# Kernel optimization log

Measured on AMD Instinct MI355X. Metric: run time of the kernel, lower is better.

Reference implementation:

```python
import jax, jax.numpy as jnp
import numpy as np

B, S, D, H = 4, 1024, 1024, 16
DH = D // H
RD = float(np.sqrt(D))


def linear_vdp(mu_a, var_a, mu_b, var_b):
    # Product of two independent random matrices: E[AB], Var[AB] (elementwise)
    mean = mu_a @ mu_b
    var = var_a @ var_b + var_a @ (mu_b ** 2) + (mu_a ** 2) @ var_b
    return mean, var


def softmax_vdp(a, var_a):
    # p = softmax(a); variance via squared Jacobian J_ij = p_i(delta_ij - p_j):
    # var_out_i = p_i^2 * (sum_j p_j^2 var_j + var_i * (1 - 2 p_i))
    p = jax.nn.softmax(a, axis=-1)
    s = jnp.sum(p * p * var_a, axis=-1, keepdims=True)
    var_out = p * p * (s + var_a * (1.0 - 2.0 * p))
    return p, var_out


def setup_inputs() -> dict:
    key = jax.random.key(0)
    ks = jax.random.split(key, 8)
    x = jax.random.normal(ks[0], (B, S, D), dtype=jnp.float32)
    var_x = jax.random.uniform(ks[1], (B, S, D), dtype=jnp.float32) * 0.1
    k = jax.random.normal(ks[2], (B, H, S, DH), dtype=jnp.float32)
    var_k = jax.random.uniform(ks[3], (B, H, S, DH), dtype=jnp.float32) * 0.1
    v = jax.random.normal(ks[4], (B, H, S, DH), dtype=jnp.float32)
    var_v = jax.random.uniform(ks[5], (B, H, S, DH), dtype=jnp.float32) * 0.1
    # LinearVDP(d, d, bias=False): weight mean + (positive) weight variance
    Wq_mu = jax.random.normal(ks[6], (D, D), dtype=jnp.float32) / np.sqrt(D)
    Wq_var = jax.random.uniform(ks[7], (D, D), dtype=jnp.float32) * (0.1 / D)
    return {"x": x, "var_x": var_x, "k": k, "var_k": var_k, "v": v,
            "var_v": var_v, "Wq_mu": Wq_mu, "Wq_var": Wq_var}


def reference(x, var_x, k, var_k, v, var_v, Wq_mu, Wq_var):
    # LinearVDP projection (y = x W^T with random weight)
    q = x @ Wq_mu.T
    var_q = var_x @ Wq_var.T + var_x @ (Wq_mu ** 2).T + (x ** 2) @ Wq_var.T
    # split heads: [B,S,D] -> [B,H,S,DH]
    q = q.reshape(B, S, H, DH).transpose(0, 2, 1, 3)
    var_q = var_q.reshape(B, S, H, DH).transpose(0, 2, 1, 3)
    # scores with variance propagation
    a, var_a = linear_vdp(q, var_q, jnp.swapaxes(k, 2, 3), jnp.swapaxes(var_k, 2, 3))
    a = a / RD
    var_a = var_a / (RD ** 2)
    # causal mask (-inf above diagonal) on the mean path only
    causal = jnp.triu(jnp.ones((S, S), dtype=bool), k=1)
    a = jnp.where(causal, -jnp.inf, a)
    a, var_a = softmax_vdp(a, var_a)
    # attention * values with variance propagation
    a, var_a = linear_vdp(a, var_a, v, var_v)
    # merge heads: [B,H,S,DH] -> [B,S,D]
    a = a.transpose(0, 2, 1, 3).reshape(B, S, D)
    var_a = var_a.transpose(0, 2, 1, 3).reshape(B, S, D)
    return x + a, var_a
```

## Files before the change

kernel.cpp:

```cpp
#include <hip/hip_runtime.h>
#include <hip/hip_bf16.h>
#include <math.h>

#define NB 4
#define NS 1024
#define ND 1024
#define NH 16
#define NDH 64
#define M4 4194304
#define M1 1048576

typedef float f16v __attribute__((ext_vector_type(16)));
typedef short bf8 __attribute__((ext_vector_type(8)));
typedef unsigned short ushort_t;

union U8 { bf8 v; unsigned u[4]; unsigned short s[8]; };

__device__ __forceinline__ unsigned pk(float lo, float hi) {
    __hip_bfloat162 h2 = __float22bfloat162_rn(make_float2(lo, hi));
    return *reinterpret_cast<unsigned*>(&h2);
}
__device__ __forceinline__ unsigned short f2b(float f) {
    unsigned u = __float_as_uint(f);
    unsigned r = (u + 0x7fffu + ((u >> 16) & 1u)) >> 16;
    return (unsigned short)r;
}
__device__ __forceinline__ float b2f(unsigned short h) {
    return __uint_as_float(((unsigned)h) << 16);
}
__device__ __forceinline__ f16v zero16() {
    f16v z;
    #pragma unroll
    for (int i = 0; i < 16; ++i) z[i] = 0.f;
    return z;
}
__device__ __forceinline__ void vscale(f16v& v, float s) {
    #pragma unroll
    for (int i = 0; i < 16; ++i) v[i] *= s;
}

__device__ __forceinline__ void gl_lds16(const ushort_t* g, ushort_t* l) {
    __builtin_amdgcn_global_load_lds(
        (const __attribute__((address_space(1))) unsigned int*)g,
        (__attribute__((address_space(3))) unsigned int*)l,
        16, 0, 0);
}

__device__ __forceinline__ bf8 mkB(unsigned p0, unsigned p1, unsigned p2, unsigned p3, int h) {
    unsigned own0 = h ? p2 : p0;
    unsigned own1 = h ? p3 : p1;
    unsigned ct0  = h ? p0 : p2;
    unsigned ct1  = h ? p1 : p3;
    unsigned x0 = (unsigned)__shfl_xor((int)ct0, 32);
    unsigned x1 = (unsigned)__shfl_xor((int)ct1, 32);
    U8 B;
    B.u[0] = h ? x0 : own0;
    B.u[1] = h ? x1 : own1;
    B.u[2] = h ? own0 : x0;
    B.u[3] = h ? own1 : x1;
    return B.v;
}


__global__ __launch_bounds__(256)
void prep_all(const float* __restrict__ x, const float* __restrict__ vx,
              const float* __restrict__ K,  const float* __restrict__ VK,
              const float* __restrict__ Vv, const float* __restrict__ VV,
              const float* __restrict__ Wm, const float* __restrict__ Wv,
              ushort_t* __restrict__ kmF, ushort_t* __restrict__ k2F, ushort_t* __restrict__ kvF,
              ushort_t* __restrict__ vmF, ushort_t* __restrict__ wF,  ushort_t* __restrict__ vvF,
              ushort_t* __restrict__ fx, ushort_t* __restrict__ fvx, ushort_t* __restrict__ fx2,
              ushort_t* __restrict__ fm, ushort_t* __restrict__ fw2, ushort_t* __restrict__ fv)
{
    __shared__ ushort_t Lm[2048], Lw[2048], Lv[2048];
    const int tid = threadIdx.x;
    const int bid = blockIdx.x;

    if (bid < 2048) {
        const int bh = bid >> 5, s = bid & 31;
        const int jp  = tid >> 3;
        const int dh0 = (tid & 7) * 8;
        const size_t gin = ((size_t)bh * NS + s * 32 + jp) * NDH + dh0;
        const size_t sbase = ((size_t)bh * 32 + s) * 2048;

        float kk[8], uu[8], vm[8], vv[8];
        *(float4*)(kk)   = *(const float4*)(K  + gin); *(float4*)(kk+4) = *(const float4*)(K  + gin + 4);
        *(float4*)(uu)   = *(const float4*)(VK + gin); *(float4*)(uu+4) = *(const float4*)(VK + gin + 4);
        *(float4*)(vm)   = *(const float4*)(Vv + gin); *(float4*)(vm+4) = *(const float4*)(Vv + gin + 4);
        *(float4*)(vv)   = *(const float4*)(VV + gin); *(float4*)(vv+4) = *(const float4*)(VV + gin + 4);

        const size_t kout = sbase + (size_t)((tid & 7) >> 1) * 512
                          + (jp + 32 * ((tid & 7) & 1)) * 8;
        unsigned o0[4], o1[4], o2[4];
        #pragma unroll
        for (int t = 0; t < 4; ++t) {
            o0[t] = pk(kk[2*t], kk[2*t+1]);
            o1[t] = pk(fmaf(kk[2*t],kk[2*t],uu[2*t]), fmaf(kk[2*t+1],kk[2*t+1],uu[2*t+1]));
            o2[t] = pk(uu[2*t], uu[2*t+1]);
        }
        *(uint4*)(kmF + kout) = make_uint4(o0[0],o0[1],o0[2],o0[3]);
        *(uint4*)(k2F + kout) = make_uint4(o1[0],o1[1],o1[2],o1[3]);
        *(uint4*)(kvF + kout) = make_uint4(o2[0],o2[1],o2[2],o2[3]);

        #pragma unroll
        for (int e = 0; e < 8; ++e) {
            const int dh = dh0 + e;
            const int idx = ((dh >> 5) * 2 + (jp >> 4)) * 512
                          + ((dh & 31) + 32 * ((jp >> 3) & 1)) * 8 + (jp & 7);
            Lm[idx] = f2b(vm[e]);
            Lw[idx] = f2b(fmaf(vm[e], vm[e], vv[e]));
            Lv[idx] = f2b(vv[e]);
        }
        __syncthreads();
        const size_t vout = sbase + (size_t)tid * 8;
        *(uint4*)(vmF + vout) = *(const uint4*)(Lm + tid * 8);
        *(uint4*)(wF  + vout) = *(const uint4*)(Lw + tid * 8);
        *(uint4*)(vvF + vout) = *(const uint4*)(Lv + tid * 8);
    } else {
        const size_t g = (size_t)(bid - 2048) * 256 + tid;
        if (g < 524288) {
            const size_t g0 = g * 8;
            const int row = (int)(g0 >> 10), k0 = (int)(g0 & 1023);
            const size_t fo = ((size_t)(row >> 5) * 64 + (k0 >> 4)) * 512
                            + ((row & 31) + 32 * ((k0 >> 3) & 1)) * 8;
            float a[8], c[8];
            *(float4*)(a)   = *(const float4*)(x + g0);  *(float4*)(a+4) = *(const float4*)(x + g0 + 4);
            *(float4*)(c)   = *(const float4*)(vx + g0); *(float4*)(c+4) = *(const float4*)(vx + g0 + 4);
            *(uint4*)(fx  + fo) = make_uint4(pk(a[0],a[1]), pk(a[2],a[3]), pk(a[4],a[5]), pk(a[6],a[7]));
            *(uint4*)(fvx + fo) = make_uint4(pk(c[0],c[1]), pk(c[2],c[3]), pk(c[4],c[5]), pk(c[6],c[7]));
            *(uint4*)(fx2 + fo) = make_uint4(pk(a[0]*a[0],a[1]*a[1]), pk(a[2]*a[2],a[3]*a[3]),
                                             pk(a[4]*a[4],a[5]*a[5]), pk(a[6]*a[6],a[7]*a[7]));
        } else {
            const size_t g0 = (g - 524288) * 8;
            const int row = (int)(g0 >> 10), k0 = (int)(g0 & 1023);
            const size_t fo = ((size_t)(row >> 5) * 64 + (k0 >> 4)) * 512
                            + ((row & 31) + 32 * ((k0 >> 3) & 1)) * 8;
            float a[8], c[8];
            *(float4*)(a)   = *(const float4*)(Wm + g0); *(float4*)(a+4) = *(const float4*)(Wm + g0 + 4);
            *(float4*)(c)   = *(const float4*)(Wv + g0); *(float4*)(c+4) = *(const float4*)(Wv + g0 + 4);
            *(uint4*)(fm  + fo) = make_uint4(pk(a[0],a[1]), pk(a[2],a[3]), pk(a[4],a[5]), pk(a[6],a[7]));
            *(uint4*)(fv  + fo) = make_uint4(pk(c[0],c[1]), pk(c[2],c[3]), pk(c[4],c[5]), pk(c[6],c[7]));
            *(uint4*)(fw2 + fo) = make_uint4(pk(fmaf(a[0],a[0],c[0]), fmaf(a[1],a[1],c[1])),
                                             pk(fmaf(a[2],a[2],c[2]), fmaf(a[3],a[3],c[3])),
                                             pk(fmaf(a[4],a[4],c[4]), fmaf(a[5],a[5],c[5])),
                                             pk(fmaf(a[6],a[6],c[6]), fmaf(a[7],a[7],c[7])));
        }
    }
}

__global__ __launch_bounds__(256, 2)
void qproj_b(const ushort_t* __restrict__ xplanes,
             const ushort_t* __restrict__ wplanes,
             ushort_t* __restrict__ qmF, ushort_t* __restrict__ vqF)
{
    __shared__ ushort_t wstg[3][12 * 512];

    const int tid  = threadIdx.x;
    const int w    = tid >> 6;
    const int lane = tid & 63;
    const int lh   = lane & 31;
    const int h    = lane >> 5;
    const int head = blockIdx.x;
    const int mb   = blockIdx.y;
    const int mt   = mb * 4 + w;
    const int nt   = head * 2 + (w & 1);

    f16v aQ0 = zero16(), aQ1 = zero16(), aV0 = zero16(), aV1 = zero16();

    const ushort_t* xb = xplanes + (size_t)mt * 64 * 512 + lane * 8;
    const ushort_t* wsrc = wplanes + ((size_t)nt * 64 + (w >> 1)) * 512 + lane * 8;

    #pragma unroll
    for (int q = 0; q < 3; ++q)
        gl_lds16(wsrc + (size_t)q * M1, &wstg[0][(3 * w + q) * 512 + lane * 8]);
    #pragma unroll
    for (int q = 0; q < 3; ++q)
        gl_lds16(wsrc + (size_t)q * M1 + 2 * 512, &wstg[1][(3 * w + q) * 512 + lane * 8]);

    for (int t = 0; t < 32; ++t) {
        const int cur = t % 3;
        if (t + 2 < 32) {
            const int nxt = (t + 2) % 3;
            #pragma unroll
            for (int q = 0; q < 3; ++q)
                gl_lds16(wsrc + (size_t)q * M1 + (size_t)(2 * (t + 2)) * 512,
                         &wstg[nxt][(3 * w + q) * 512 + lane * 8]);
            asm volatile("s_waitcnt vmcnt(6)" ::: "memory");
        } else if (t + 1 < 32) {
            asm volatile("s_waitcnt vmcnt(3)" ::: "memory");
        } else {
            asm volatile("s_waitcnt vmcnt(0)" ::: "memory");
        }
        __builtin_amdgcn_s_barrier();
        __builtin_amdgcn_sched_barrier(0);

        const ushort_t* sc = wstg[cur];
        #pragma unroll
        for (int kcL = 0; kcL < 2; ++kcL) {
            const int off = (2 * t + kcL) * 512;
            bf8 bx  = *(const bf8*)(xb + 0 * (size_t)M4 + off);
            bf8 bvx = *(const bf8*)(xb + 1 * (size_t)M4 + off);
            bf8 bx2 = *(const bf8*)(xb + 2 * (size_t)M4 + off);
            bf8 A0m = *(const bf8*)(sc + (3 * (2 * kcL + 0) + 0) * 512 + lane * 8);
            bf8 A0w = *(const bf8*)(sc + (3 * (2 * kcL + 0) + 1) * 512 + lane * 8);
            bf8 A0v = *(const bf8*)(sc + (3 * (2 * kcL + 0) + 2) * 512 + lane * 8);
            bf8 A1m = *(const bf8*)(sc + (3 * (2 * kcL + 1) + 0) * 512 + lane * 8);
            bf8 A1w = *(const bf8*)(sc + (3 * (2 * kcL + 1) + 1) * 512 + lane * 8);
            bf8 A1v = *(const bf8*)(sc + (3 * (2 * kcL + 1) + 2) * 512 + lane * 8);
            aQ0 = __builtin_amdgcn_mfma_f32_32x32x16_bf16(A0m, bx,  aQ0, 0, 0, 0);
            aV0 = __builtin_amdgcn_mfma_f32_32x32x16_bf16(A0w, bvx, aV0, 0, 0, 0);
            aV0 = __builtin_amdgcn_mfma_f32_32x32x16_bf16(A0v, bx2, aV0, 0, 0, 0);
            aQ1 = __builtin_amdgcn_mfma_f32_32x32x16_bf16(A1m, bx,  aQ1, 0, 0, 0);
            aV1 = __builtin_amdgcn_mfma_f32_32x32x16_bf16(A1w, bvx, aV1, 0, 0, 0);
            aV1 = __builtin_amdgcn_mfma_f32_32x32x16_bf16(A1v, bx2, aV1, 0, 0, 0);
        }
        __builtin_amdgcn_sched_barrier(0);
        __builtin_amdgcn_s_barrier();
    }

    const int mrow = mt * 32 + lh;
    const int b = mrow >> 10;
    const int rt = mt & 31;
    const size_t bh_base = ((size_t)(b * NH + head)) * 65536 + (size_t)rt * 2048;
    const float S1 = 0.03125f, S2 = 0.0009765625f;
    #pragma unroll
    for (int i = 0; i < 16; i += 2) {
        const int dh0 = (i & 3) + 8 * (i >> 2) + 4 * h;
        const size_t o = bh_base + (size_t)(dh0 >> 4) * 512
                       + (lh + 32 * ((dh0 >> 3) & 1)) * 8 + (dh0 & 7);
        *(unsigned*)(qmF + o)         = pk(aQ0[i]*S1, aQ0[i+1]*S1);
        *(unsigned*)(qmF + o + 1024)  = pk(aQ1[i]*S1, aQ1[i+1]*S1);
        *(unsigned*)(vqF + o)         = pk(aV0[i]*S2, aV0[i+1]*S2);
        *(unsigned*)(vqF + o + 1024)  = pk(aV1[i]*S2, aV1[i+1]*S2);
    }
}

__global__ __launch_bounds__(256, 2)
void attn_b(const ushort_t* __restrict__ qmF, const ushort_t* __restrict__ vqF,
            const ushort_t* __restrict__ planes,
            const float* __restrict__ x,
            float* __restrict__ out0, float* __restrict__ out1)
{
    __shared__ union {
        ushort_t stg[3][6 * 2048];
        float ep[128][66];
    } sm;

    const int tid  = threadIdx.x;
    const int w    = tid >> 6;
    const int lane = tid & 63;
    const int lh   = lane & 31;
    const int h    = lane >> 5;
    const int blk  = blockIdx.x;
    const int lb   = (blk & 7) * 64 + (blk >> 3);
    const int rb   = 7 - (lb & 7);
    const int bh   = lb >> 3;
    const int rt   = rb * 4 + w;
    const size_t base = (size_t)bh * 65536;

    bf8 fqm[4], fvq[4], fq2[4];
    {
        const ushort_t* qp = qmF + base + (size_t)rt * 2048 + lane * 8;
        const ushort_t* vp = vqF + base + (size_t)rt * 2048 + lane * 8;
        #pragma unroll
        for (int c = 0; c < 4; ++c) {
            fqm[c] = *(const bf8*)(qp + c * 512);
            fvq[c] = *(const bf8*)(vp + c * 512);
            U8 t; t.v = fqm[c];
            U8 r;
            #pragma unroll
            for (int k = 0; k < 4; ++k) {
                float q0 = b2f(t.s[2*k]), q1 = b2f(t.s[2*k+1]);
                r.u[k] = pk(q0*q0, q1*q1);
            }
            fq2[c] = r.v;
        }
    }

    f16v aN1[2], aN2w[2], aM2[2], aN3[2];
    #pragma unroll
    for (int dt = 0; dt < 2; ++dt) { aN1[dt]=zero16(); aN2w[dt]=zero16(); aM2[dt]=zero16(); aN3[dt]=zero16(); }
    float mrun = -INFINITY, Zrun = 0.f, S2run = 0.f;

    const int nstage = 4 * rb + 4;
    #pragma unroll
    for (int p = 0; p < 6; ++p)
        gl_lds16(planes + (size_t)p * M4 + base + w * 512 + lane * 8,
                 &sm.stg[0][p * 2048 + w * 512 + lane * 8]);
    #pragma unroll
    for (int p = 0; p < 6; ++p)
        gl_lds16(planes + (size_t)p * M4 + base + 2048 + w * 512 + lane * 8,
                 &sm.stg[1][p * 2048 + w * 512 + lane * 8]);

    for (int st = 0; st < nstage; ++st) {
        const int cur = st % 3;
        if (st + 2 < nstage) {
            const int nxt = (st + 2) % 3;
            #pragma unroll
            for (int p = 0; p < 6; ++p)
                gl_lds16(planes + (size_t)p * M4 + base + (size_t)(st + 2) * 2048 + w * 512 + lane * 8,
                         &sm.stg[nxt][p * 2048 + w * 512 + lane * 8]);
            asm volatile("s_waitcnt vmcnt(12)" ::: "memory");
        } else if (st + 1 < nstage) {
            asm volatile("s_waitcnt vmcnt(6)" ::: "memory");
        } else {
            asm volatile("s_waitcnt vmcnt(0)" ::: "memory");
        }
        __builtin_amdgcn_s_barrier();
        __builtin_amdgcn_sched_barrier(0);

        if (st <= rt) {
            const ushort_t* sb = sm.stg[cur];
            f16v accA = zero16(), accU = zero16();
            #pragma unroll
            for (int c = 0; c < 4; ++c) {
                bf8 A0 = *(const bf8*)(sb + 0 * 2048 + c * 512 + lane * 8);
                bf8 A1 = *(const bf8*)(sb + 1 * 2048 + c * 512 + lane * 8);
                bf8 A2 = *(const bf8*)(sb + 2 * 2048 + c * 512 + lane * 8);
                accA = __builtin_amdgcn_mfma_f32_32x32x16_bf16(A0, fqm[c], accA, 0, 0, 0);
                accU = __builtin_amdgcn_mfma_f32_32x32x16_bf16(A1, fvq[c], accU, 0, 0, 0);
                accU = __builtin_amdgcn_mfma_f32_32x32x16_bf16(A2, fq2[c], accU, 0, 0, 0);
            }
            if (st == rt) {
                #pragma unroll
                for (int i = 0; i < 16; ++i) {
                    const int jl = (i & 3) + 8 * (i >> 2) + 4 * h;
                    if (jl > lh) accA[i] = -INFINITY;
                }
            }
            float mx = accA[0];
            #pragma unroll
            for (int i = 1; i < 16; ++i) mx = fmaxf(mx, accA[i]);
            mx = fmaxf(mx, __shfl_xor(mx, 32));
            if (!__all(mx <= mrun + 8.f)) {
                const float mnew = fmaxf(mrun, mx);
                const float s1 = __expf(mrun - mnew);
                const float s2 = s1 * s1, s3 = s2 * s1;
                Zrun *= s1; S2run *= s2;
                #pragma unroll
                for (int dt = 0; dt < 2; ++dt) { vscale(aN1[dt],s1); vscale(aN2w[dt],s2); vscale(aM2[dt],s2); vscale(aN3[dt],s3); }
                mrun = mnew;
            }
            float Zt = 0.f, St = 0.f;
            #pragma unroll
            for (int i = 0; i < 16; ++i) {
                const float e = __expf(accA[i] - mrun);
                accA[i] = e;
                Zt += e; St = fmaf(e * e, accU[i], St);
            }
            Zt += __shfl_xor(Zt, 32); St += __shfl_xor(St, 32);
            Zrun += Zt; S2run += St;

            #pragma unroll
            for (int c2 = 0; c2 < 2; ++c2) {
                unsigned pE[4], pE2[4], pEU[4], pE3[4];
                #pragma unroll
                for (int k = 0; k < 4; ++k) {
                    const int i0 = 8*c2 + 2*k;
                    const float e0 = accA[i0], e1 = accA[i0+1];
                    const float q0 = e0*e0, q1 = e1*e1;
                    const float t0 = q0*accU[i0], t1 = q1*accU[i0+1];
                    pE [k] = pk(e0, e1);
                    pE2[k] = pk(q0, q1);
                    pEU[k] = pk(t0, t1);
                    pE3[k] = pk(t0*e0, t1*e1);
                }
                bf8 BE  = mkB(pE [0], pE [1], pE [2], pE [3], h);
                bf8 BE2 = mkB(pE2[0], pE2[1], pE2[2], pE2[3], h);
                bf8 BEU = mkB(pEU[0], pEU[1], pEU[2], pEU[3], h);
                bf8 BE3 = mkB(pE3[0], pE3[1], pE3[2], pE3[3], h);
                #pragma unroll
                for (int dt = 0; dt < 2; ++dt) {
                    const ushort_t* vp = sb + 3 * 2048 + (dt * 2 + c2) * 512 + lane * 8;
                    bf8 Am = *(const bf8*)(vp + 0 * 2048);
                    bf8 Aw = *(const bf8*)(vp + 1 * 2048);
                    bf8 Av = *(const bf8*)(vp + 2 * 2048);
                    aN1[dt]  = __builtin_amdgcn_mfma_f32_32x32x16_bf16(Am, BE,  aN1[dt],  0, 0, 0);
                    aN2w[dt] = __builtin_amdgcn_mfma_f32_32x32x16_bf16(Aw, BE2, aN2w[dt], 0, 0, 0);
                    aM2[dt]  = __builtin_amdgcn_mfma_f32_32x32x16_bf16(Aw, BEU, aM2[dt],  0, 0, 0);
                    aM2[dt]  = __builtin_amdgcn_mfma_f32_32x32x16_bf16(Av, BE2, aM2[dt],  0, 0, 0);
                    aN3[dt]  = __builtin_amdgcn_mfma_f32_32x32x16_bf16(Aw, BE3, aN3[dt],  0, 0, 0);
                }
            }
        }
        __builtin_amdgcn_sched_barrier(0);
        __builtin_amdgcn_s_barrier();
    }

    const float rZ  = 1.f / Zrun;
    const float rZ2 = rZ * rZ;
    const float sS  = S2run * rZ2;
    const int b = bh >> 4, head = bh & 15;

    #pragma unroll
    for (int dt = 0; dt < 2; ++dt)
        #pragma unroll
        for (int i = 0; i < 16; ++i) {
            const int col = 32*dt + (i & 3) + 8*(i >> 2) + 4*h;
            sm.ep[w*32 + lh][col] = aN1[dt][i] * rZ;
        }
    __syncthreads();
    {
        const int row = tid >> 1, half = (tid & 1) * 32;
        const size_t o = ((size_t)b * NS + rb*128 + row) * ND + head * NDH + half;
        #pragma unroll
        for (int q4 = 0; q4 < 32; q4 += 4) {
            float4 t = make_float4(sm.ep[row][half+q4], sm.ep[row][half+q4+1],
                                   sm.ep[row][half+q4+2], sm.ep[row][half+q4+3]);
            float4 xi = *(const float4*)(x + o + q4);
            *(float4*)(out0 + o + q4) = make_float4(t.x+xi.x, t.y+xi.y, t.z+xi.z, t.w+xi.w);
        }
    }
    __syncthreads();
    #pragma unroll
    for (int dt = 0; dt < 2; ++dt)
        #pragma unroll
        for (int i = 0; i < 16; ++i) {
            const int col = 32*dt + (i & 3) + 8*(i >> 2) + 4*h;
            sm.ep[w*32 + lh][col] = rZ2 * fmaf(sS, aN2w[dt][i], aM2[dt][i]) - 2.f*rZ2*rZ*aN3[dt][i];
        }
    __syncthreads();
    {
        const int row = tid >> 1, half = (tid & 1) * 32;
        const size_t o = ((size_t)b * NS + rb*128 + row) * ND + head * NDH + half;
        #pragma unroll
        for (int q4 = 0; q4 < 32; q4 += 4) {
            float4 t = make_float4(sm.ep[row][half+q4], sm.ep[row][half+q4+1],
                                   sm.ep[row][half+q4+2], sm.ep[row][half+q4+3]);
            *(float4*)(out1 + o + q4) = t;
        }
    }
}

extern "C" void kernel_launch(void* const* d_in, const int* in_sizes, int n_in,
                              void* d_out, int out_size, void* d_ws, size_t ws_size,
                              hipStream_t stream)
{
    (void)in_sizes; (void)n_in; (void)out_size; (void)ws_size;
    const float* x  = (const float*)d_in[0];
    const float* vx = (const float*)d_in[1];
    const float* K  = (const float*)d_in[2];
    const float* VK = (const float*)d_in[3];
    const float* Vv = (const float*)d_in[4];
    const float* VV = (const float*)d_in[5];
    const float* Wm = (const float*)d_in[6];
    const float* Wv = (const float*)d_in[7];

    float* out0 = (float*)d_out;
    float* out1 = out0 + (size_t)NB * NS * ND;

    ushort_t* qm  = (ushort_t*)d_ws;
    ushort_t* vq  = qm  + M4;
    ushort_t* kmF = vq  + M4;
    ushort_t* k2F = kmF + M4;
    ushort_t* kvF = k2F + M4;
    ushort_t* vmF = kvF + M4;
    ushort_t* wF  = vmF + M4;
    ushort_t* vvF = wF  + M4;
    ushort_t* fxF = vvF + M4;
    ushort_t* fvxF= fxF + M4;
    ushort_t* fx2F= fvxF+ M4;
    ushort_t* fmF = fx2F+ M4;
    ushort_t* fw2F= fmF + M1;
    ushort_t* fvF = fw2F+ M1;

    prep_all<<<4608, 256, 0, stream>>>(x, vx, K, VK, Vv, VV, Wm, Wv,
                                       kmF, k2F, kvF, vmF, wF, vvF,
                                       fxF, fvxF, fx2F, fmF, fw2F, fvF);
    qproj_b<<<dim3(NH, 32), 256, 0, stream>>>(fxF, fmF, qm, vq);
    attn_b<<<512, 256, 0, stream>>>(qm, vq, kmF, x, out0, out1);
}
```

Before: 168.4 us.

## Restructure pipeline barriers, prefetch x operands to registers, tree-reduce softmax

In the projection kernel, the x operand fragments for the next k-step are loaded into registers one iteration ahead. The two barriers per iteration become one barrier placed before the prefetch issue, with vmcnt waits retuned to match. The attention kernel likewise drops its trailing barrier, adds s_setprio around the MFMA sections, and turns the serial max, sum and variance reductions into tree reductions to shorten dependency chains. This aims to cut barrier stalls and global-load latency on the critical path, at the cost of more registers and a tricky wait-count/LDS-reuse correctness argument.

```diff
diff --git a/kernel.cpp b/kernel.cpp
--- a/kernel.cpp
+++ b/kernel.cpp
@@ -177,30 +177,40 @@
     for (int q = 0; q < 3; ++q)
         gl_lds16(wsrc + (size_t)q * M1 + 2 * 512, &wstg[1][(3 * w + q) * 512 + lane * 8]);
 
+    bf8 xc[6], xn[6];
+    #pragma unroll
+    for (int kcL = 0; kcL < 2; ++kcL)
+        #pragma unroll
+        for (int q = 0; q < 3; ++q)
+            xc[3 * kcL + q] = *(const bf8*)(xb + (size_t)q * M4 + kcL * 512);
+
     for (int t = 0; t < 32; ++t) {
         const int cur = t % 3;
+        if (t < 31) asm volatile("s_waitcnt vmcnt(9)" ::: "memory");
+        else        asm volatile("s_waitcnt vmcnt(6)" ::: "memory");
+        __builtin_amdgcn_s_barrier();
         if (t + 2 < 32) {
             const int nxt = (t + 2) % 3;
             #pragma unroll
             for (int q = 0; q < 3; ++q)
                 gl_lds16(wsrc + (size_t)q * M1 + (size_t)(2 * (t + 2)) * 512,
                          &wstg[nxt][(3 * w + q) * 512 + lane * 8]);
-            asm volatile("s_waitcnt vmcnt(6)" ::: "memory");
-        } else if (t + 1 < 32) {
-            asm volatile("s_waitcnt vmcnt(3)" ::: "memory");
-        } else {
-            asm volatile("s_waitcnt vmcnt(0)" ::: "memory");
-        }
-        __builtin_amdgcn_s_barrier();
+        }
         __builtin_amdgcn_sched_barrier(0);
-
+        if (t + 1 < 32) {
+            #pragma unroll
+            for (int kcL = 0; kcL < 2; ++kcL)
+                #pragma unroll
+                for (int q = 0; q < 3; ++q)
+                    xn[3 * kcL + q] = *(const bf8*)(xb + (size_t)q * M4 + (2 * (t + 1) + kcL) * 512);
+        }
         const ushort_t* sc = wstg[cur];
+        __builtin_amdgcn_s_setprio(1);
         #pragma unroll
         for (int kcL = 0; kcL < 2; ++kcL) {
-            const int off = (2 * t + kcL) * 512;
-            bf8 bx  = *(const bf8*)(xb + 0 * (size_t)M4 + off);
-            bf8 bvx = *(const bf8*)(xb + 1 * (size_t)M4 + off);
-            bf8 bx2 = *(const bf8*)(xb + 2 * (size_t)M4 + off);
+            bf8 bx  = xc[3 * kcL + 0];
+            bf8 bvx = xc[3 * kcL + 1];
+            bf8 bx2 = xc[3 * kcL + 2];
             bf8 A0m = *(const bf8*)(sc + (3 * (2 * kcL + 0) + 0) * 512 + lane * 8);
             bf8 A0w = *(const bf8*)(sc + (3 * (2 * kcL + 0) + 1) * 512 + lane * 8);
             bf8 A0v = *(const bf8*)(sc + (3 * (2 * kcL + 0) + 2) * 512 + lane * 8);
@@ -214,8 +224,11 @@
             aV1 = __builtin_amdgcn_mfma_f32_32x32x16_bf16(A1w, bvx, aV1, 0, 0, 0);
             aV1 = __builtin_amdgcn_mfma_f32_32x32x16_bf16(A1v, bx2, aV1, 0, 0, 0);
         }
+        __builtin_amdgcn_s_setprio(0);
+        asm volatile("s_waitcnt lgkmcnt(0)" ::: "memory");
         __builtin_amdgcn_sched_barrier(0);
-        __builtin_amdgcn_s_barrier();
+        #pragma unroll
+        for (int q = 0; q < 6; ++q) xc[q] = xn[q];
     }
 
     const int mrow = mt * 32 + lh;
@@ -294,22 +307,20 @@
 
     for (int st = 0; st < nstage; ++st) {
         const int cur = st % 3;
+        if (st + 1 < nstage) asm volatile("s_waitcnt vmcnt(6)" ::: "memory");
+        else                 asm volatile("s_waitcnt vmcnt(0)" ::: "memory");
+        __builtin_amdgcn_s_barrier();
         if (st + 2 < nstage) {
             const int nxt = (st + 2) % 3;
             #pragma unroll
             for (int p = 0; p < 6; ++p)
                 gl_lds16(planes + (size_t)p * M4 + base + (size_t)(st + 2) * 2048 + w * 512 + lane * 8,
                          &sm.stg[nxt][p * 2048 + w * 512 + lane * 8]);
-            asm volatile("s_waitcnt vmcnt(12)" ::: "memory");
-        } else if (st + 1 < nstage) {
-            asm volatile("s_waitcnt vmcnt(6)" ::: "memory");
-        } else {
-            asm volatile("s_waitcnt vmcnt(0)" ::: "memory");
-        }
-        __builtin_amdgcn_s_barrier();
+        }
         __builtin_amdgcn_sched_barrier(0);
 
         if (st <= rt) {
+            __builtin_amdgcn_s_setprio(1);
             const ushort_t* sb = sm.stg[cur];
             f16v accA = zero16(), accU = zero16();
             #pragma unroll
@@ -328,9 +339,12 @@
                     if (jl > lh) accA[i] = -INFINITY;
                 }
             }
-            float mx = accA[0];
-            #pragma unroll
-            for (int i = 1; i < 16; ++i) mx = fmaxf(mx, accA[i]);
+            float t8[8];
+            #pragma unroll
+            for (int i = 0; i < 8; ++i) t8[i] = fmaxf(accA[i], accA[i + 8]);
+            #pragma unroll
+            for (int i = 0; i < 4; ++i) t8[i] = fmaxf(t8[i], t8[i + 4]);
+            float mx = fmaxf(fmaxf(t8[0], t8[1]), fmaxf(t8[2], t8[3]));
             mx = fmaxf(mx, __shfl_xor(mx, 32));
             if (!__all(mx <= mrun + 8.f)) {
                 const float mnew = fmaxf(mrun, mx);
@@ -341,13 +355,19 @@
                 for (int dt = 0; dt < 2; ++dt) { vscale(aN1[dt],s1); vscale(aN2w[dt],s2); vscale(aM2[dt],s2); vscale(aN3[dt],s3); }
                 mrun = mnew;
             }
-            float Zt = 0.f, St = 0.f;
-            #pragma unroll
-            for (int i = 0; i < 16; ++i) {
-                const float e = __expf(accA[i] - mrun);
-                accA[i] = e;
-                Zt += e; St = fmaf(e * e, accU[i], St);
-            }
+            float zt[8], sq[8];
+            #pragma unroll
+            for (int i = 0; i < 16; ++i) accA[i] = __expf(accA[i] - mrun);
+            #pragma unroll
+            for (int i = 0; i < 8; ++i) {
+                zt[i] = accA[i] + accA[i + 8];
+                sq[i] = fmaf(accA[i] * accA[i], accU[i],
+                             accA[i + 8] * accA[i + 8] * accU[i + 8]);
+            }
+            #pragma unroll
+            for (int i = 0; i < 4; ++i) { zt[i] += zt[i + 4]; sq[i] += sq[i + 4]; }
+            float Zt = (zt[0] + zt[1]) + (zt[2] + zt[3]);
+            float St = (sq[0] + sq[1]) + (sq[2] + sq[3]);
             Zt += __shfl_xor(Zt, 32); St += __shfl_xor(St, 32);
             Zrun += Zt; S2run += St;
 
@@ -382,10 +402,12 @@
                     aN3[dt]  = __builtin_amdgcn_mfma_f32_32x32x16_bf16(Aw, BE3, aN3[dt],  0, 0, 0);
                 }
             }
-        }
-        __builtin_amdgcn_sched_barrier(0);
-        __builtin_amdgcn_s_barrier();
-    }
+            __builtin_amdgcn_s_setprio(0);
+            asm volatile("s_waitcnt lgkmcnt(0)" ::: "memory");
+            __builtin_amdgcn_sched_barrier(0);
+        }
+    }
+    __syncthreads();
 
     const float rZ  = 1.f / Zrun;
     const float rZ2 = rZ * rZ;
```

Measured after the change: 170.0 us. About the same (+1.0%).
